# Performance work log

Measured on AMD Instinct MI355X. Metric: run time of the kernel, lower is better.

## Reference

```python
import jax, jax.numpy as jnp
import numpy as np

NUM_HEADS = 8
NUM_POINTS = 4


def _bilinear_gather(vl, loc, h, w):
    """MSDeformAttn bilinear sampling (align_corners=False, zero padding).
    vl: (BN, h*w, H, D) one level's values; loc: (BN, Q, H, P, 2) normalized [0,1].
    Returns (BN, Q, H, P, D)."""
    BN, _, H, D = vl.shape
    Q, P = loc.shape[1], loc.shape[3]
    x = loc[..., 0] * w - 0.5
    y = loc[..., 1] * h - 0.5
    x0 = jnp.floor(x); y0 = jnp.floor(y)
    lx = x - x0; ly = y - y0
    x0i = x0.astype(jnp.int32); y0i = y0.astype(jnp.int32)
    x1i = x0i + 1; y1i = y0i + 1
    vt = vl.transpose(0, 2, 1, 3)  # (BN, H, hw, D)

    def gather(yi, xi):
        valid = (yi >= 0) & (yi < h) & (xi >= 0) & (xi < w)
        idx = jnp.clip(yi, 0, h - 1) * w + jnp.clip(xi, 0, w - 1)  # (BN,Q,H,P)
        idx_t = idx.transpose(0, 2, 1, 3).reshape(BN, H, Q * P)
        g = jnp.take_along_axis(vt, idx_t[..., None], axis=2)  # (BN,H,QP,D)
        g = g.reshape(BN, H, Q, P, D).transpose(0, 2, 1, 3, 4)
        return jnp.where(valid[..., None], g, jnp.zeros((), vl.dtype))

    w00 = ((1 - ly) * (1 - lx))[..., None]
    w01 = ((1 - ly) * lx)[..., None]
    w10 = (ly * (1 - lx))[..., None]
    w11 = (ly * lx)[..., None]
    return (gather(y0i, x0i) * w00 + gather(y0i, x1i) * w01
            + gather(y1i, x0i) * w10 + gather(y1i, x1i) * w11)


def _forward(query, value, reference_points, query_mask, spatial_shapes, level_start_index,
             Wv, bv, Woff, boff, Watt, batt, Wo, bo):
    B, Z, Y, X, C = query.shape
    Q = Z * Y * X
    BN = value.shape[0]
    N = BN // B  # cameras per sample (uniform lengths)
    H, P = NUM_HEADS, NUM_POINTS
    shapes = np.asarray(spatial_shapes)  # static level shapes
    starts = np.asarray(level_start_index)
    L = shapes.shape[0]
    D = C // H
    mask = query_mask.astype(query.dtype)  # (BN, Q)
    # expand each sample's voxel queries to its N cameras
    qf = jnp.broadcast_to(query.reshape(B, 1, Q, C), (B, N, Q, C)).reshape(BN, Q, C)
    v = (value @ Wv + bv).reshape(BN, -1, H, D)
    off = (qf @ Woff + boff).reshape(BN, Q, H, L, P, 2)
    aw = jax.nn.softmax((qf @ Watt + batt).reshape(BN, Q, H, L * P), axis=-1)
    aw = aw.reshape(BN, Q, H, L, P)
    # offset_normalizer = (w, h) per level
    normalizer = jnp.asarray(np.stack([shapes[:, 1], shapes[:, 0]], -1), query.dtype)
    loc = reference_points[:, :, None, None, None, :] + off / normalizer[None, None, None, :, None, :]
    out = jnp.zeros((BN, Q, H, D), query.dtype)
    for l in range(L):
        h, w = int(shapes[l, 0]), int(shapes[l, 1])
        s = int(starts[l])
        vl = v[:, s:s + h * w]
        sampled = _bilinear_gather(vl, loc[:, :, :, l], h, w)  # (BN,Q,H,P,D)
        out = out + jnp.einsum('bqhpd,bqhp->bqhd', sampled, aw[:, :, :, l])
    attn = out.reshape(BN, Q, C) @ Wo + bo
    # identity + attn, then rebatch_mask_sequence zeroes non-masked voxels
    full = (qf + attn) * mask[..., None]
    summed = full.reshape(B, N, Q, C).sum(axis=1)
    counts = jnp.maximum(mask.reshape(B, N, Q).sum(axis=1), 1.0)
    return (summed / counts[..., None]).reshape(B, Z, Y, X, C)


def setup_inputs() -> dict:
    key = jax.random.key(0)
    ks = jax.random.split(key, 9)
    B, N = 2, 4
    Z, Y, X, C = 8, 32, 32, 256
    Q = Z * Y * X
    BN = B * N
    shapes = np.array([[64, 112], [32, 56], [16, 28], [8, 14]], np.int64)
    starts = np.concatenate([[0], np.cumsum(shapes[:, 0] * shapes[:, 1])[:-1]]).astype(np.int64)
    Nv = int((shapes[:, 0] * shapes[:, 1]).sum())  # 9520
    H, L, P = NUM_HEADS, shapes.shape[0], NUM_POINTS
    s = 0.02
    return dict(
        query=jax.random.normal(ks[0], (B, Z, Y, X, C), jnp.float32),
        value=jax.random.normal(ks[1], (BN, Nv, C), jnp.float32),
        reference_points=jax.random.uniform(ks[2], (BN, Q, 2), jnp.float32),
        query_mask=jax.random.bernoulli(ks[3], 0.6, (BN, Q)),
        spatial_shapes=jnp.asarray(shapes),
        level_start_index=jnp.asarray(starts),
        Wv=jax.random.normal(ks[4], (C, C), jnp.float32) * s,
        bv=jnp.zeros((C,), jnp.float32),
        Woff=jax.random.normal(ks[5], (C, H * L * P * 2), jnp.float32) * s,
        boff=jax.random.normal(ks[6], (H * L * P * 2,), jnp.float32),
        Watt=jax.random.normal(ks[7], (C, H * L * P), jnp.float32) * s,
        batt=jnp.zeros((H * L * P,), jnp.float32),
        Wo=jax.random.normal(ks[8], (C, C), jnp.float32) * s,
        bo=jnp.zeros((C,), jnp.float32),
    )


def reference(query, value, reference_points, query_mask, spatial_shapes, level_start_index,
              Wv, bv, Woff, boff, Watt, batt, Wo, bo):
    return _forward(query, value, reference_points, query_mask, spatial_shapes, level_start_index,
                    Wv, bv, Woff, boff, Watt, batt, Wo, bo)
```

## Files before the change

kernel.cpp:

```cpp
#include <hip/hip_runtime.h>
#include <cstdint>
#include <cstddef>

#define QQ 8192
#define CDIM 256
#define NV 9520
#define NLVL 4
#define NPTS 4
#define NHEAD 8

typedef __attribute__((ext_vector_type(8))) short short8;
typedef __attribute__((ext_vector_type(4))) float f32x4;

__device__ __forceinline__ unsigned short f2bf(float f)
{
    unsigned u = __float_as_uint(f);
    unsigned r = (u + 0x7fffu + ((u >> 16) & 1u)) >> 16;
    return (unsigned short)r;
}
__device__ __forceinline__ unsigned pk2bf(float a, float b)
{
    return (unsigned)f2bf(a) | ((unsigned)f2bf(b) << 16);
}

__global__ void pack_weights_kernel(
    const float* __restrict__ Wv,
    const float* __restrict__ Woff, const float* __restrict__ boff,
    const float* __restrict__ Watt, const float* __restrict__ batt,
    const float* __restrict__ Wo,
    unsigned short* __restrict__ Wt_v,
    unsigned short* __restrict__ Wt_oa,
    unsigned short* __restrict__ Wt_o,
    float* __restrict__ bias_oa)
{
    const int n = blockIdx.x, k = threadIdx.x;
    if (n < 256) {
        Wt_v[n * 256 + k] = f2bf(Wv[(size_t)k * 256 + n]);
    } else if (n < 512) {
        const int c = n - 256;
        Wt_oa[c * 256 + k] = f2bf(Woff[(size_t)k * 256 + c]);
        if (k == 0) bias_oa[c] = boff[c];
    } else if (n < 640) {
        const int c = n - 512;
        Wt_oa[(256 + c) * 256 + k] = f2bf(Watt[(size_t)k * 128 + c]);
        if (k == 0) bias_oa[256 + c] = batt[c];
    } else {
        const int c = n - 640;
        Wt_o[c * 256 + k] = f2bf(Wo[(size_t)k * 256 + c]);
    }
}

enum { EP_BIAS_BF16 = 0, EP_BIAS_F32 = 1, EP_WO_FINAL = 2 };

template <int EP, bool AF32>
__global__ __launch_bounds__(256) void mfma_gemm_kernel(
    const void* __restrict__ Ap,
    const unsigned short* __restrict__ Bt,
    const float* __restrict__ bias,
    void* __restrict__ C, int ldc,
    const float* __restrict__ query,
    const float* __restrict__ bo,
    const float* __restrict__ cnts)
{
    __shared__ unsigned short As[128 * 64];
    __shared__ unsigned short Bs[128 * 64];
    const int tid  = threadIdx.x;
    const int lane = tid & 63;
    const int wave = tid >> 6;
    const int wm = wave >> 1, wn = wave & 1;
    const int lr = lane & 15, g = lane >> 4;
    const int m0 = blockIdx.x * 128, n0 = blockIdx.y * 128;

    f32x4 acc[4][4];
    #pragma unroll
    for (int mi = 0; mi < 4; ++mi)
        #pragma unroll
        for (int ni = 0; ni < 4; ++ni)
            acc[mi][ni] = (f32x4){0.f, 0.f, 0.f, 0.f};

    const unsigned short* gB = Bt + (size_t)n0 * 256;

    for (int kt = 0; kt < 4; ++kt) {
        uint4 ra[4], rb[4];
        #pragma unroll
        for (int it = 0; it < 4; ++it) {
            const int fb  = it * 256 + tid;
            const int row = fb >> 3, kb = fb & 7;
            if constexpr (AF32) {
                const float* gA = (const float*)Ap + (size_t)m0 * 256;
                const float* p = gA + (size_t)row * 256 + kt * 64 + kb * 8;
                float4 f0 = *(const float4*)p;
                float4 f1 = *(const float4*)(p + 4);
                ra[it] = make_uint4(pk2bf(f0.x, f0.y), pk2bf(f0.z, f0.w),
                                    pk2bf(f1.x, f1.y), pk2bf(f1.z, f1.w));
            } else {
                const unsigned short* gA = (const unsigned short*)Ap + (size_t)m0 * 256;
                ra[it] = *(const uint4*)(gA + (size_t)row * 256 + kt * 64 + kb * 8);
            }
            rb[it] = *(const uint4*)(gB + (size_t)row * 256 + kt * 64 + kb * 8);
        }
        __syncthreads();
        #pragma unroll
        for (int it = 0; it < 4; ++it) {
            const int fb  = it * 256 + tid;
            const int row = fb >> 3, kb = fb & 7;
            const int sw  = (kb ^ (row & 7)) << 3;
            *(uint4*)&As[row * 64 + sw] = ra[it];
            *(uint4*)&Bs[row * 64 + sw] = rb[it];
        }
        __syncthreads();
        #pragma unroll
        for (int kk = 0; kk < 2; ++kk) {
            const int kb = kk * 4 + g;
            short8 af[4], bf[4];
            #pragma unroll
            for (int mi = 0; mi < 4; ++mi) {
                const int row = wm * 64 + mi * 16 + lr;
                af[mi] = *(const short8*)&As[row * 64 + ((kb ^ (row & 7)) << 3)];
            }
            #pragma unroll
            for (int ni = 0; ni < 4; ++ni) {
                const int row = wn * 64 + ni * 16 + lr;
                bf[ni] = *(const short8*)&Bs[row * 64 + ((kb ^ (row & 7)) << 3)];
            }
            #pragma unroll
            for (int mi = 0; mi < 4; ++mi)
                #pragma unroll
                for (int ni = 0; ni < 4; ++ni)
                    acc[mi][ni] = __builtin_amdgcn_mfma_f32_16x16x32_bf16(
                        af[mi], bf[ni], acc[mi][ni], 0, 0, 0);
        }
    }

    if constexpr (EP == EP_BIAS_BF16 || EP == EP_BIAS_F32) {
        float bcol[4];
        #pragma unroll
        for (int ni = 0; ni < 4; ++ni)
            bcol[ni] = bias[n0 + wn * 64 + ni * 16 + lr];
        #pragma unroll
        for (int mi = 0; mi < 4; ++mi) {
            #pragma unroll
            for (int j = 0; j < 4; ++j) {
                const int gm = m0 + wm * 64 + mi * 16 + g * 4 + j;
                #pragma unroll
                for (int ni = 0; ni < 4; ++ni) {
                    const int gn = n0 + wn * 64 + ni * 16 + lr;
                    const float r = acc[mi][ni][j] + bcol[ni];
                    if constexpr (EP == EP_BIAS_BF16)
                        ((unsigned short*)C)[(size_t)gm * ldc + gn] = f2bf(r);
                    else
                        ((float*)C)[(size_t)gm * ldc + gn] = r;
                }
            }
        }
    } else {
        float bcol[4];
        #pragma unroll
        for (int ni = 0; ni < 4; ++ni)
            bcol[ni] = bo[n0 + wn * 64 + ni * 16 + lr];
        #pragma unroll
        for (int mi = 0; mi < 4; ++mi) {
            #pragma unroll
            for (int j = 0; j < 4; ++j) {
                const int gm = m0 + wm * 64 + mi * 16 + g * 4 + j;
                const float sm = cnts[gm];
                const float inv = 1.f / fmaxf(sm, 1.f);
                #pragma unroll
                for (int ni = 0; ni < 4; ++ni) {
                    const int gn = n0 + wn * 64 + ni * 16 + lr;
                    const float qv = query[(size_t)gm * CDIM + gn] + bcol[ni];
                    ((float*)C)[(size_t)gm * ldc + gn] =
                        (sm * qv + acc[mi][ni][j]) * inv;
                }
            }
        }
    }
}

__global__ void detect_mask_kernel(const unsigned int* __restrict__ m, int* flag)
{
    __shared__ int notI32, notF32;
    if (threadIdx.x == 0) { notI32 = 0; notF32 = 0; }
    __syncthreads();
    for (int i = threadIdx.x; i < 1024; i += 256) {
        unsigned v = m[i];
        if (v > 1u) notI32 = 1;
        if (v != 0u && v != 0x3F800000u) notF32 = 1;
    }
    __syncthreads();
    if (threadIdx.x == 0) *flag = (!notI32) ? 1 : ((!notF32) ? 2 : 0);
}

__device__ __forceinline__ float read_mask(const void* p, int f, size_t i)
{
    if (f == 1) return (float)((const int*)p)[i];
    if (f == 2) return ((const float*)p)[i];
    return (float)((const unsigned char*)p)[i];
}

__global__ __launch_bounds__(256) void sample_reduce_kernel(
    const unsigned short* __restrict__ v,
    const float* __restrict__ offatt,
    const float* __restrict__ refp,
    const void* __restrict__ maskp,
    const int* __restrict__ flag,
    unsigned short* __restrict__ S,
    float* __restrict__ cnts)
{
    __shared__ int4   sidx[4][NHEAD][17];
    __shared__ float4 swt[4][NHEAD][17];
    __shared__ float  red[4][CDIM];
    __shared__ float  smv[4];
    const int tid  = threadIdx.x;
    const int wn   = tid >> 6;
    const int lane = tid & 63;
    const int bq   = blockIdx.x;
    const int b    = bq >> 13;
    const int q    = bq & (QQ - 1);
    const int bn   = b * 4 + wn;

    const float mn = read_mask(maskp, *flag, (size_t)bn * QQ + q);
    if (lane == 0) smv[wn] = mn;

    const float* oa = offatt + (size_t)bq * 384;
    const float rx = refp[((size_t)bn * QQ + q) * 2 + 0];
    const float ry = refp[((size_t)bn * QQ + q) * 2 + 1];

    #pragma unroll
    for (int cc = 0; cc < 2; ++cc) {
        const int c = lane + cc * 64;
        const int hcomb = c >> 4;
        const int pcomb = c & 15;
        const int l = (c >> 2) & 3;
        const int hh = 64 >> l;
        const int ww = 112 >> l;
        const int s  = (l > 0 ? 7168 : 0) + (l > 1 ? 1792 : 0) + (l > 2 ? 448 : 0);
        const float offx = oa[c * 2 + 0];
        const float offy = oa[c * 2 + 1];
        const float logit = oa[256 + c];
        float mx = logit;
        #pragma unroll
        for (int d = 1; d < 16; d <<= 1) mx = fmaxf(mx, __shfl_xor(mx, d));
        const float e = __expf(logit - mx);
        float se = e;
        #pragma unroll
        for (int d = 1; d < 16; d <<= 1) se += __shfl_xor(se, d);
        const float aw = e / se;

        const float x = rx * (float)ww - 0.5f + offx;
        const float y = ry * (float)hh - 0.5f + offy;
        const float x0f = floorf(x), y0f = floorf(y);
        const float lx = x - x0f, ly = y - y0f;
        const int x0 = (int)x0f, y0 = (int)y0f;
        const int x1 = x0 + 1,  y1 = y0 + 1;
        const bool vx0 = (x0 >= 0) & (x0 < ww);
        const bool vx1 = (x1 >= 0) & (x1 < ww);
        const bool vy0 = (y0 >= 0) & (y0 < hh);
        const bool vy1 = (y1 >= 0) & (y1 < hh);
        const int xc0 = min(max(x0, 0), ww - 1);
        const int xc1 = min(max(x1, 0), ww - 1);
        const int yc0 = min(max(y0, 0), hh - 1);
        const int yc1 = min(max(y1, 0), hh - 1);
        float w00 = (1.f - ly) * (1.f - lx) * aw;
        float w01 = (1.f - ly) * lx * aw;
        float w10 = ly * (1.f - lx) * aw;
        float w11 = ly * lx * aw;
        w00 = (vy0 & vx0) ? w00 : 0.f;
        w01 = (vy0 & vx1) ? w01 : 0.f;
        w10 = (vy1 & vx0) ? w10 : 0.f;
        w11 = (vy1 & vx1) ? w11 : 0.f;
        sidx[wn][hcomb][pcomb] = make_int4(s + yc0 * ww + xc0, s + yc0 * ww + xc1,
                                           s + yc1 * ww + xc0, s + yc1 * ww + xc1);
        swt[wn][hcomb][pcomb]  = make_float4(w00, w01, w10, w11);
    }
    __syncthreads();

    const int half = lane >> 5;
    const int h8   = (lane >> 2) & 7;
    const int dq   = lane & 3;
    float acc[8] = {0.f, 0.f, 0.f, 0.f, 0.f, 0.f, 0.f, 0.f};
    if (mn != 0.f) {
        const uint4* vb = (const uint4*)(v + (size_t)bn * NV * CDIM);
        const int lo = h8 * 4 + dq;
        #pragma unroll 8
        for (int p = 0; p < 16; ++p) {
            const int4   id = sidx[wn][h8][p];
            const float4 wt = swt[wn][h8][p];
            const int   pixA = half ? id.y : id.x;
            const float wA   = half ? wt.y : wt.x;
            const int   pixB = half ? id.w : id.z;
            const float wB   = half ? wt.w : wt.z;
            const uint4 gA = vb[(size_t)(pixA * 32 + lo)];
            const uint4 gB = vb[(size_t)(pixB * 32 + lo)];
            #define BFLO(u) __uint_as_float((u) << 16)
            #define BFHI(u) __uint_as_float((u) & 0xffff0000u)
            acc[0] += wA * BFLO(gA.x) + wB * BFLO(gB.x);
            acc[1] += wA * BFHI(gA.x) + wB * BFHI(gB.x);
            acc[2] += wA * BFLO(gA.y) + wB * BFLO(gB.y);
            acc[3] += wA * BFHI(gA.y) + wB * BFHI(gB.y);
            acc[4] += wA * BFLO(gA.z) + wB * BFLO(gB.z);
            acc[5] += wA * BFHI(gA.z) + wB * BFHI(gB.z);
            acc[6] += wA * BFLO(gA.w) + wB * BFLO(gB.w);
            acc[7] += wA * BFHI(gA.w) + wB * BFHI(gB.w);
            #undef BFLO
            #undef BFHI
        }
    }
    #pragma unroll
    for (int j = 0; j < 8; ++j) acc[j] += __shfl_xor(acc[j], 32);
    if (half == 0) {
        const int ch = h8 * 32 + dq * 8;
        *(float4*)&red[wn][ch]     = make_float4(acc[0], acc[1], acc[2], acc[3]);
        *(float4*)&red[wn][ch + 4] = make_float4(acc[4], acc[5], acc[6], acc[7]);
    }
    __syncthreads();

    const float ssum = red[0][tid] + red[1][tid] + red[2][tid] + red[3][tid];
    S[(size_t)bq * CDIM + tid] = f2bf(ssum);
    if (tid == 0) cnts[bq] = smv[0] + smv[1] + smv[2] + smv[3];
}

extern "C" void kernel_launch(void* const* d_in, const int* in_sizes, int n_in,
                              void* d_out, int out_size, void* d_ws, size_t ws_size,
                              hipStream_t stream)
{
    (void)in_sizes; (void)n_in; (void)out_size; (void)ws_size;
    const float* query = (const float*)d_in[0];
    const float* value = (const float*)d_in[1];
    const float* refp  = (const float*)d_in[2];
    const void*  maskp = d_in[3];
    const float* Wv    = (const float*)d_in[6];
    const float* bv    = (const float*)d_in[7];
    const float* Woff  = (const float*)d_in[8];
    const float* boff  = (const float*)d_in[9];
    const float* Watt  = (const float*)d_in[10];
    const float* batt  = (const float*)d_in[11];
    const float* Wo    = (const float*)d_in[12];
    const float* bo    = (const float*)d_in[13];
    float* out = (float*)d_out;
    char* ws = (char*)d_ws;

    unsigned short* v_proj  = (unsigned short*)(ws + 0);
    float*          offatt  = (float*)(ws + 38993920);
    unsigned short* S_bf16  = (unsigned short*)(ws + 64159744);
    unsigned short* Wt_v    = (unsigned short*)(ws + 72548352);
    unsigned short* Wt_oa   = (unsigned short*)(ws + 72679424);
    unsigned short* Wt_o    = (unsigned short*)(ws + 72876032);
    float*          bias_oa = (float*)(ws + 73007104);
    float*          cnts    = (float*)(ws + 73008640);
    int*            flag    = (int*)(ws + 73074176);

    detect_mask_kernel<<<1, 256, 0, stream>>>((const unsigned int*)maskp, flag);

    pack_weights_kernel<<<896, 256, 0, stream>>>(
        Wv, Woff, boff, Watt, batt, Wo, Wt_v, Wt_oa, Wt_o, bias_oa);

    mfma_gemm_kernel<EP_BIAS_BF16, true><<<dim3(595, 2), 256, 0, stream>>>(
        value, Wt_v, bv, v_proj, CDIM, nullptr, nullptr, nullptr);

    mfma_gemm_kernel<EP_BIAS_F32, true><<<dim3(128, 3), 256, 0, stream>>>(
        query, Wt_oa, bias_oa, offatt, 384, nullptr, nullptr, nullptr);

    sample_reduce_kernel<<<16384, 256, 0, stream>>>(
        v_proj, offatt, refp, maskp, flag, S_bf16, cnts);

    mfma_gemm_kernel<EP_WO_FINAL, false><<<dim3(128, 2), 256, 0, stream>>>(
        S_bf16, Wt_o, nullptr, out, CDIM, query, bo, cnts);
}
```

Baseline: 220.0 us.

## Use full-width 128x256 GEMM tiles and per-wave four-corner bilinear gather

Adds a 512-thread GEMM kernel whose tile covers all 256 output columns, so each A row block (including the fp32 value tensor) is loaded and converted once instead of once per column tile. Both the value projection and the output projection now use it. The sampling kernel is restructured so each lane gathers all four bilinear corners for its head and channel slice with 8-byte loads. This removes the half-wave split, the cross-half shuffle reduction and one block barrier. In exchange the GEMM uses more LDS and registers per block, which lowers occupancy. Dropping the barrier relies on the index and weight tables being written and read within the same wave.

Result: no change. 218.5 us (-0.7%).

```diff
diff --git a/kernel.cpp b/kernel.cpp
--- a/kernel.cpp
+++ b/kernel.cpp
@@ -132,45 +132,143 @@
         }
     }
 
-    if constexpr (EP == EP_BIAS_BF16 || EP == EP_BIAS_F32) {
-        float bcol[4];
+    float bcol[4];
+    #pragma unroll
+    for (int ni = 0; ni < 4; ++ni)
+        bcol[ni] = bias[n0 + wn * 64 + ni * 16 + lr];
+    #pragma unroll
+    for (int mi = 0; mi < 4; ++mi) {
+        #pragma unroll
+        for (int j = 0; j < 4; ++j) {
+            const int gm = m0 + wm * 64 + mi * 16 + g * 4 + j;
+            #pragma unroll
+            for (int ni = 0; ni < 4; ++ni) {
+                const int gn = n0 + wn * 64 + ni * 16 + lr;
+                const float r = acc[mi][ni][j] + bcol[ni];
+                if constexpr (EP == EP_BIAS_BF16)
+                    ((unsigned short*)C)[(size_t)gm * ldc + gn] = f2bf(r);
+                else
+                    ((float*)C)[(size_t)gm * ldc + gn] = r;
+            }
+        }
+    }
+}
+
+template <int EP, bool AF32>
+__global__ __launch_bounds__(512) void mfma_gemm256_kernel(
+    const void* __restrict__ Ap,
+    const unsigned short* __restrict__ Bt,
+    const float* __restrict__ bias,
+    void* __restrict__ C,
+    const float* __restrict__ query,
+    const float* __restrict__ bo,
+    const float* __restrict__ cnts)
+{
+    __shared__ unsigned short As[128 * 64];
+    __shared__ unsigned short Bs[256 * 64];
+    const int tid  = threadIdx.x;
+    const int lane = tid & 63;
+    const int wave = tid >> 6;
+    const int wm = wave >> 2, wn = wave & 3;
+    const int lr = lane & 15, g = lane >> 4;
+    const int m0 = blockIdx.x * 128;
+
+    f32x4 acc[4][4];
+    #pragma unroll
+    for (int mi = 0; mi < 4; ++mi)
         #pragma unroll
         for (int ni = 0; ni < 4; ++ni)
-            bcol[ni] = bias[n0 + wn * 64 + ni * 16 + lr];
-        #pragma unroll
-        for (int mi = 0; mi < 4; ++mi) {
-            #pragma unroll
-            for (int j = 0; j < 4; ++j) {
-                const int gm = m0 + wm * 64 + mi * 16 + g * 4 + j;
+            acc[mi][ni] = (f32x4){0.f, 0.f, 0.f, 0.f};
+
+    for (int kt = 0; kt < 4; ++kt) {
+        uint4 ra[2], rb[4];
+        #pragma unroll
+        for (int it = 0; it < 2; ++it) {
+            const int fb  = it * 512 + tid;
+            const int row = fb >> 3, kb = fb & 7;
+            if constexpr (AF32) {
+                const float* gA = (const float*)Ap + (size_t)m0 * 256;
+                const float* p = gA + (size_t)row * 256 + kt * 64 + kb * 8;
+                float4 f0 = *(const float4*)p;
+                float4 f1 = *(const float4*)(p + 4);
+                ra[it] = make_uint4(pk2bf(f0.x, f0.y), pk2bf(f0.z, f0.w),
+                                    pk2bf(f1.x, f1.y), pk2bf(f1.z, f1.w));
+            } else {
+                const unsigned short* gA = (const unsigned short*)Ap + (size_t)m0 * 256;
+                ra[it] = *(const uint4*)(gA + (size_t)row * 256 + kt * 64 + kb * 8);
+            }
+        }
+        #pragma unroll
+        for (int it = 0; it < 4; ++it) {
+            const int fb  = it * 512 + tid;
+            const int row = fb >> 3, kb = fb & 7;
+            rb[it] = *(const uint4*)(Bt + (size_t)row * 256 + kt * 64 + kb * 8);
+        }
+        __syncthreads();
+        #pragma unroll
+        for (int it = 0; it < 2; ++it) {
+            const int fb  = it * 512 + tid;
+            const int row = fb >> 3, kb = fb & 7;
+            *(uint4*)&As[row * 64 + ((kb ^ (row & 7)) << 3)] = ra[it];
+        }
+        #pragma unroll
+        for (int it = 0; it < 4; ++it) {
+            const int fb  = it * 512 + tid;
+            const int row = fb >> 3, kb = fb & 7;
+            *(uint4*)&Bs[row * 64 + ((kb ^ (row & 7)) << 3)] = rb[it];
+        }
+        __syncthreads();
+        #pragma unroll
+        for (int kk = 0; kk < 2; ++kk) {
+            const int kb = kk * 4 + g;
+            short8 af[4], bf[4];
+            #pragma unroll
+            for (int mi = 0; mi < 4; ++mi) {
+                const int row = wm * 64 + mi * 16 + lr;
+                af[mi] = *(const short8*)&As[row * 64 + ((kb ^ (row & 7)) << 3)];
+            }
+            #pragma unroll
+            for (int ni = 0; ni < 4; ++ni) {
+                const int row = wn * 64 + ni * 16 + lr;
+                bf[ni] = *(const short8*)&Bs[row * 64 + ((kb ^ (row & 7)) << 3)];
+            }
+            #pragma unroll
+            for (int mi = 0; mi < 4; ++mi)
                 #pragma unroll
-                for (int ni = 0; ni < 4; ++ni) {
-                    const int gn = n0 + wn * 64 + ni * 16 + lr;
-                    const float r = acc[mi][ni][j] + bcol[ni];
-                    if constexpr (EP == EP_BIAS_BF16)
-                        ((unsigned short*)C)[(size_t)gm * ldc + gn] = f2bf(r);
-                    else
-                        ((float*)C)[(size_t)gm * ldc + gn] = r;
-                }
-            }
-        }
-    } else {
-        float bcol[4];
-        #pragma unroll
-        for (int ni = 0; ni < 4; ++ni)
-            bcol[ni] = bo[n0 + wn * 64 + ni * 16 + lr];
-        #pragma unroll
-        for (int mi = 0; mi < 4; ++mi) {
-            #pragma unroll
-            for (int j = 0; j < 4; ++j) {
-                const int gm = m0 + wm * 64 + mi * 16 + g * 4 + j;
+                for (int ni = 0; ni < 4; ++ni)
+                    acc[mi][ni] = __builtin_amdgcn_mfma_f32_16x16x32_bf16(
+                        af[mi], bf[ni], acc[mi][ni], 0, 0, 0);
+        }
+    }
+
+    float bcol[4];
+    #pragma unroll
+    for (int ni = 0; ni < 4; ++ni)
+        bcol[ni] = (EP == EP_WO_FINAL ? bo : bias)[wn * 64 + ni * 16 + lr];
+    #pragma unroll
+    for (int mi = 0; mi < 4; ++mi) {
+        #pragma unroll
+        for (int j = 0; j < 4; ++j) {
+            const int gm = m0 + wm * 64 + mi * 16 + g * 4 + j;
+            if constexpr (EP == EP_WO_FINAL) {
                 const float sm = cnts[gm];
                 const float inv = 1.f / fmaxf(sm, 1.f);
                 #pragma unroll
                 for (int ni = 0; ni < 4; ++ni) {
-                    const int gn = n0 + wn * 64 + ni * 16 + lr;
+                    const int gn = wn * 64 + ni * 16 + lr;
                     const float qv = query[(size_t)gm * CDIM + gn] + bcol[ni];
-                    ((float*)C)[(size_t)gm * ldc + gn] =
+                    ((float*)C)[(size_t)gm * CDIM + gn] =
                         (sm * qv + acc[mi][ni][j]) * inv;
+                }
+            } else {
+                #pragma unroll
+                for (int ni = 0; ni < 4; ++ni) {
+                    const int gn = wn * 64 + ni * 16 + lr;
+                    const float r = acc[mi][ni][j] + bcol[ni];
+                    if constexpr (EP == EP_BIAS_BF16)
+                        ((unsigned short*)C)[(size_t)gm * CDIM + gn] = f2bf(r);
+                    else
+                        ((float*)C)[(size_t)gm * CDIM + gn] = r;
                 }
             }
         }
@@ -273,46 +371,32 @@
                                            s + yc1 * ww + xc0, s + yc1 * ww + xc1);
         swt[wn][hcomb][pcomb]  = make_float4(w00, w01, w10, w11);
     }
-    __syncthreads();
-
-    const int half = lane >> 5;
-    const int h8   = (lane >> 2) & 7;
-    const int dq   = lane & 3;
-    float acc[8] = {0.f, 0.f, 0.f, 0.f, 0.f, 0.f, 0.f, 0.f};
+
+    float4 acc = make_float4(0.f, 0.f, 0.f, 0.f);
     if (mn != 0.f) {
-        const uint4* vb = (const uint4*)(v + (size_t)bn * NV * CDIM);
-        const int lo = h8 * 4 + dq;
-        #pragma unroll 8
+        const int h  = lane >> 3;
+        const int d4 = lane & 7;
+        const int laneoff = h * 8 + d4;
+        const uint2* vb = (const uint2*)(v + (size_t)bn * NV * CDIM);
+        #pragma unroll 4
         for (int p = 0; p < 16; ++p) {
-            const int4   id = sidx[wn][h8][p];
-            const float4 wt = swt[wn][h8][p];
-            const int   pixA = half ? id.y : id.x;
-            const float wA   = half ? wt.y : wt.x;
-            const int   pixB = half ? id.w : id.z;
-            const float wB   = half ? wt.w : wt.z;
-            const uint4 gA = vb[(size_t)(pixA * 32 + lo)];
-            const uint4 gB = vb[(size_t)(pixB * 32 + lo)];
+            const int4   id = sidx[wn][h][p];
+            const float4 wt = swt[wn][h][p];
+            const uint2 g00 = vb[(size_t)(id.x * 64 + laneoff)];
+            const uint2 g01 = vb[(size_t)(id.y * 64 + laneoff)];
+            const uint2 g10 = vb[(size_t)(id.z * 64 + laneoff)];
+            const uint2 g11 = vb[(size_t)(id.w * 64 + laneoff)];
             #define BFLO(u) __uint_as_float((u) << 16)
             #define BFHI(u) __uint_as_float((u) & 0xffff0000u)
-            acc[0] += wA * BFLO(gA.x) + wB * BFLO(gB.x);
-            acc[1] += wA * BFHI(gA.x) + wB * BFHI(gB.x);
-            acc[2] += wA * BFLO(gA.y) + wB * BFLO(gB.y);
-            acc[3] += wA * BFHI(gA.y) + wB * BFHI(gB.y);
-            acc[4] += wA * BFLO(gA.z) + wB * BFLO(gB.z);
-            acc[5] += wA * BFHI(gA.z) + wB * BFHI(gB.z);
-            acc[6] += wA * BFLO(gA.w) + wB * BFLO(gB.w);
-            acc[7] += wA * BFHI(gA.w) + wB * BFHI(gB.w);
+            acc.x += wt.x * BFLO(g00.x) + wt.y * BFLO(g01.x) + wt.z * BFLO(g10.x) + wt.w * BFLO(g11.x);
+            acc.y += wt.x * BFHI(g00.x) + wt.y * BFHI(g01.x) + wt.z * BFHI(g10.x) + wt.w * BFHI(g11.x);
+            acc.z += wt.x * BFLO(g00.y) + wt.y * BFLO(g01.y) + wt.z * BFLO(g10.y) + wt.w * BFLO(g11.y);
+            acc.w += wt.x * BFHI(g00.y) + wt.y * BFHI(g01.y) + wt.z * BFHI(g10.y) + wt.w * BFHI(g11.y);
             #undef BFLO
             #undef BFHI
         }
     }
-    #pragma unroll
-    for (int j = 0; j < 8; ++j) acc[j] += __shfl_xor(acc[j], 32);
-    if (half == 0) {
-        const int ch = h8 * 32 + dq * 8;
-        *(float4*)&red[wn][ch]     = make_float4(acc[0], acc[1], acc[2], acc[3]);
-        *(float4*)&red[wn][ch + 4] = make_float4(acc[4], acc[5], acc[6], acc[7]);
-    }
+    *(float4*)&red[wn][lane * 4] = acc;
     __syncthreads();
 
     const float ssum = red[0][tid] + red[1][tid] + red[2][tid] + red[3][tid];
@@ -355,8 +439,8 @@
     pack_weights_kernel<<<896, 256, 0, stream>>>(
         Wv, Woff, boff, Watt, batt, Wo, Wt_v, Wt_oa, Wt_o, bias_oa);
 
-    mfma_gemm_kernel<EP_BIAS_BF16, true><<<dim3(595, 2), 256, 0, stream>>>(
-        value, Wt_v, bv, v_proj, CDIM, nullptr, nullptr, nullptr);
+    mfma_gemm256_kernel<EP_BIAS_BF16, true><<<595, 512, 0, stream>>>(
+        value, Wt_v, bv, v_proj, nullptr, nullptr, nullptr);
 
     mfma_gemm_kernel<EP_BIAS_F32, true><<<dim3(128, 3), 256, 0, stream>>>(
         query, Wt_oa, bias_oa, offatt, 384, nullptr, nullptr, nullptr);
@@ -364,6 +448,6 @@
     sample_reduce_kernel<<<16384, 256, 0, stream>>>(
         v_proj, offatt, refp, maskp, flag, S_bf16, cnts);
 
-    mfma_gemm_kernel<EP_WO_FINAL, false><<<dim3(128, 2), 256, 0, stream>>>(
-        S_bf16, Wt_o, nullptr, out, CDIM, query, bo, cnts);
-}
+    mfma_gemm256_kernel<EP_WO_FINAL, false><<<128, 512, 0, stream>>>(
+        S_bf16, Wt_o, nullptr, out, query, bo, cnts);
+}
```
